# Performance work log

Hardware: AMD Instinct MI355X
Metric: run time of the kernel (lower is better)

The kernel has to match this reference:

```python
import jax, jax.numpy as jnp
import numpy as np
from jax import lax

K_KNN = 20           # DGCNN default neighborhood size
SLOPE = 0.2          # LeakyReLU negative slope


def _leaky(x):
    return jnp.where(x >= 0, x, SLOPE * x)


def _knn(x, k):
    # x: [B, N, C] -> idx [B, N, k] of nearest neighbors (incl. self) in feature space
    xx = jnp.sum(x * x, axis=-1)                       # [B, N]
    d = xx[:, :, None] + xx[:, None, :] - 2.0 * jnp.einsum('bnc,bmc->bnm', x, x)
    return lax.top_k(-d, k)[1]                          # [B, N, k]


def _edge_conv(x, idx, w, b):
    # x: [B, N, C]; idx: [B, N, k]; w: [O, 2C]; b: [O]
    neigh = jax.vmap(lambda xt, i: xt[i])(x, idx)       # [B, N, k, C]
    center = jnp.broadcast_to(x[:, :, None, :], neigh.shape)
    feat = jnp.concatenate([neigh - center, center], axis=-1)  # [B, N, k, 2C]
    h = _leaky(jnp.einsum('bnkc,oc->bnko', feat, w) + b)
    return jnp.max(h, axis=2)                           # [B, N, O]


def setup_inputs() -> dict:
    key = jax.random.key(0)
    ks = jax.random.split(key, 20)
    B, N, J, KR = 4, 4096, 24, 4
    layers = [64, 128, 256]

    def w_init(k, o, i):
        return jax.random.normal(k, (o, i), jnp.float32) / np.sqrt(i)

    inp = {
        'V': jax.random.normal(ks[0], (B, N, 3), jnp.float32),
        'W': jax.random.uniform(ks[1], (B, J, N), jnp.float32),
        'skeletonOneRingIdx': jax.random.randint(ks[2], (B, J, KR), 0, J),
    }
    # geoNet edge-conv params (input channels per layer: 3, 64, 128 -> 2C inputs)
    inp['g1_w'] = w_init(ks[3], 64, 6);    inp['g1_b'] = jnp.zeros((64,), jnp.float32)
    inp['g2_w'] = w_init(ks[4], 128, 128); inp['g2_b'] = jnp.zeros((128,), jnp.float32)
    inp['g3_w'] = w_init(ks[5], 256, 256); inp['g3_b'] = jnp.zeros((256,), jnp.float32)
    # skeleton edge-conv params (inputs: 451 -> 902, 256 -> 512, 128 -> 256)
    inp['s1_w'] = w_init(ks[6], 256, 902); inp['s1_b'] = jnp.zeros((256,), jnp.float32)
    inp['s2_w'] = w_init(ks[7], 128, 512); inp['s2_b'] = jnp.zeros((128,), jnp.float32)
    inp['s3_w'] = w_init(ks[8], 64, 256);  inp['s3_b'] = jnp.zeros((64,), jnp.float32)
    # jointMLP 1x1 convs: 448 -> 512 -> 256 -> 3
    inp['m1_w'] = w_init(ks[9], 512, 448);  inp['m1_b'] = jnp.zeros((512,), jnp.float32)
    inp['m2_w'] = w_init(ks[10], 256, 512); inp['m2_b'] = jnp.zeros((256,), jnp.float32)
    inp['m3_w'] = w_init(ks[11], 3, 256);   inp['m3_b'] = jnp.zeros((3,), jnp.float32)
    return inp


def reference(V, W, skeletonOneRingIdx,
              g1_w, g1_b, g2_w, g2_b, g3_w, g3_b,
              s1_w, s1_b, s2_w, s2_b, s3_w, s3_b,
              m1_w, m1_b, m2_w, m2_b, m3_w, m3_b):
    # ---- geoNet: DGCNN with dynamic kNN, output cat([xyz, l1, l2, l3]) -> [B, N, 451]
    outs = [V]
    h = V
    for w, b in ((g1_w, g1_b), (g2_w, g2_b), (g3_w, g3_b)):
        idx = _knn(h, K_KNN)
        h = _edge_conv(h, idx, w, b)
        outs.append(h)
    feat = jnp.concatenate(outs, axis=-1)                # [B, N, 451]

    # ---- weighted pooling onto skeleton joints
    pooled = jnp.einsum('bjn,bnc->bjc', W, feat)
    pooled = pooled / (jnp.sum(W, axis=-1, keepdims=True) + 1e-5)  # [B, J, 451]

    # ---- skeleton edge convs with fixed one-ring idx
    v1 = _edge_conv(pooled, skeletonOneRingIdx, s1_w, s1_b)  # [B, J, 256]
    v2 = _edge_conv(v1, skeletonOneRingIdx, s2_w, s2_b)      # [B, J, 128]
    v3 = _edge_conv(v2, skeletonOneRingIdx, s3_w, s3_b)      # [B, J, 64]

    joints = jnp.concatenate([v1, v2, v3], axis=-1)          # [B, J, 448]
    h = _leaky(jnp.einsum('bjc,oc->bjo', joints, m1_w) + m1_b)
    h = _leaky(jnp.einsum('bjc,oc->bjo', h, m2_w) + m2_b)
    out = jnp.einsum('bjc,oc->bjo', h, m3_w) + m3_b          # [B, J, 3]
    return out
```

## Files before the change

### kernel.cpp

```cpp
#include <hip/hip_runtime.h>
#include <hip/hip_bf16.h>
#include <float.h>

#define B_   4
#define N_   4096
#define J_   24
#define KR_  4
#define KNN_ 20
#define SLOPE 0.2f
#define SLABN 64
#define NSLAB (N_ / SLABN)
#define NTILE 32
#define SCAP 512

__global__ void k_norm(const float* __restrict__ h, float* __restrict__ xx, int C) {
    int i = blockIdx.x * blockDim.x + threadIdx.x;
    if (i >= B_ * N_) return;
    const float* hp = h + (size_t)i * C;
    float s = 0.f;
    for (int c = 0; c < C; ++c) { float v = hp[c]; s += v * v; }
    xx[i] = s;
}

__device__ __forceinline__ unsigned mapf(float f) {
    unsigned u = __float_as_uint(f);
    return (u & 0x80000000u) ? ~u : (u | 0x80000000u);
}
__device__ __forceinline__ unsigned key16(float f) {
    return mapf(f) >> 16;
}

__global__ __launch_bounds__(256) void k_dist(const float* __restrict__ Xall, int C,
                                              const float* __restrict__ xxall,
                                              unsigned short* __restrict__ Dall, int b0) {
    __shared__ float As[16][132];
    __shared__ float Bs[16][132];
    int b = b0 + blockIdx.y;
    const float* X   = Xall + (size_t)b * N_ * C;
    const float* xxb = xxall + (size_t)b * N_;
    unsigned short* D = Dall + (size_t)blockIdx.y * N_ * N_;

    int t = blockIdx.x;
    int ti = 0;
    while (t >= NTILE - ti) { t -= NTILE - ti; ++ti; }
    int tj = ti + t;
    int row0 = ti * 128, col0 = tj * 128;
    int tid = threadIdx.x;
    int tr = tid >> 4, tc = tid & 15;
    float acc[8][8] = {{0.f}};
    for (int kt = 0; kt < C; kt += 16) {
#pragma unroll
        for (int i = 0; i < 8; ++i) {
            int e = tid + 256 * i;
            int r = e >> 4, kk = e & 15;
            int gk = kt + kk;
            As[kk][r] = (gk < C) ? X[(size_t)(row0 + r) * C + gk] : 0.f;
            Bs[kk][r] = (gk < C) ? X[(size_t)(col0 + r) * C + gk] : 0.f;
        }
        __syncthreads();
#pragma unroll
        for (int kk = 0; kk < 16; ++kk) {
            float a[8], bv[8];
            *(float4*)&a[0]  = *(const float4*)&As[kk][tr * 4];
            *(float4*)&a[4]  = *(const float4*)&As[kk][64 + tr * 4];
            *(float4*)&bv[0] = *(const float4*)&Bs[kk][tc * 4];
            *(float4*)&bv[4] = *(const float4*)&Bs[kk][64 + tc * 4];
#pragma unroll
            for (int i = 0; i < 8; ++i)
#pragma unroll
                for (int j = 0; j < 8; ++j) acc[i][j] += a[i] * bv[j];
        }
        __syncthreads();
    }
    float xc[8], xr[8];
#pragma unroll
    for (int j = 0; j < 4; ++j) {
        xc[j]     = xxb[col0 + tc * 4 + j];
        xc[4 + j] = xxb[col0 + 64 + tc * 4 + j];
        xr[j]     = xxb[row0 + tr * 4 + j];
        xr[4 + j] = xxb[row0 + 64 + tr * 4 + j];
    }
#pragma unroll
    for (int i = 0; i < 8; ++i) {
        int lr = (i < 4) ? (tr * 4 + i) : (64 + tr * 4 + (i - 4));
        float xri = xr[i];
        float o0x = xri + xc[0] - 2.f * acc[i][0];
        float o0y = xri + xc[1] - 2.f * acc[i][1];
        float o0z = xri + xc[2] - 2.f * acc[i][2];
        float o0w = xri + xc[3] - 2.f * acc[i][3];
        float o1x = xri + xc[4] - 2.f * acc[i][4];
        float o1y = xri + xc[5] - 2.f * acc[i][5];
        float o1z = xri + xc[6] - 2.f * acc[i][6];
        float o1w = xri + xc[7] - 2.f * acc[i][7];
        unsigned short* dp = D + (size_t)(row0 + lr) * N_ + col0;
        uint2 w0, w1;
        w0.x = key16(o0x) | (key16(o0y) << 16);
        w0.y = key16(o0z) | (key16(o0w) << 16);
        w1.x = key16(o1x) | (key16(o1y) << 16);
        w1.y = key16(o1z) | (key16(o1w) << 16);
        *(uint2*)(dp + tc * 4)      = w0;
        *(uint2*)(dp + 64 + tc * 4) = w1;
    }
    if (ti == tj) return;
    float* tb = &As[0][0];
    for (int p = 0; p < 4; ++p) {
        __syncthreads();
        int h = p >> 1;
        int tclo = (p & 1) * 8;
        if (tc >= tclo && tc < tclo + 8) {
#pragma unroll
            for (int jj = 0; jj < 4; ++jj) {
                int j = h * 4 + jj;
                int cl = h * 64 + tc * 4 + jj - 32 * p;
                float xcj = xc[j];
                float4 vlo, vhi;
                vlo.x = xr[0] + xcj - 2.f * acc[0][j];
                vlo.y = xr[1] + xcj - 2.f * acc[1][j];
                vlo.z = xr[2] + xcj - 2.f * acc[2][j];
                vlo.w = xr[3] + xcj - 2.f * acc[3][j];
                vhi.x = xr[4] + xcj - 2.f * acc[4][j];
                vhi.y = xr[5] + xcj - 2.f * acc[5][j];
                vhi.z = xr[6] + xcj - 2.f * acc[6][j];
                vhi.w = xr[7] + xcj - 2.f * acc[7][j];
                *(float4*)&tb[cl * 132 + tr * 4]      = vlo;
                *(float4*)&tb[cl * 132 + 64 + tr * 4] = vhi;
            }
        }
        __syncthreads();
        int rl  = tid >> 3;
        int c16 = (tid & 7) * 16;
#pragma unroll
        for (int q = 0; q < 4; ++q) {
            float4 v = *(const float4*)&tb[rl * 132 + c16 + q * 4];
            uint2 ks;
            ks.x = key16(v.x) | (key16(v.y) << 16);
            ks.y = key16(v.z) | (key16(v.w) << 16);
            *(uint2*)(D + (size_t)(col0 + 32 * p + rl) * N_ + row0 + c16 + q * 4) = ks;
        }
    }
}

__device__ __forceinline__ unsigned long long shflx64(unsigned long long v, int m) {
    unsigned lo = (unsigned)v, hi = (unsigned)(v >> 32);
    lo = (unsigned)__shfl_xor((int)lo, m, 64);
    hi = (unsigned)__shfl_xor((int)hi, m, 64);
    return ((unsigned long long)hi << 32) | lo;
}

__device__ __forceinline__ float bsort64f(float v, int lane) {
#pragma unroll
    for (int k = 2; k <= 64; k <<= 1) {
#pragma unroll
        for (int j = k >> 1; j > 0; j >>= 1) {
            float o = __shfl_xor(v, j, 64);
            bool keepmin = (((lane & j) == 0) == ((lane & k) == 0));
            float mn = fminf(v, o), mx = fmaxf(v, o);
            v = keepmin ? mn : mx;
        }
    }
    return v;
}

__device__ __forceinline__ unsigned bsort64i(unsigned v, int lane) {
#pragma unroll
    for (int k = 2; k <= 64; k <<= 1) {
#pragma unroll
        for (int j = k >> 1; j > 0; j >>= 1) {
            unsigned o = (unsigned)__shfl_xor((int)v, j, 64);
            bool keepmin = (((lane & j) == 0) == ((lane & k) == 0));
            unsigned mn = (v < o) ? v : o;
            unsigned mx = (v < o) ? o : v;
            v = keepmin ? mn : mx;
        }
    }
    return v;
}

__device__ __forceinline__ unsigned long long bsort64u(unsigned long long v, int lane) {
#pragma unroll
    for (int k = 2; k <= 64; k <<= 1) {
#pragma unroll
        for (int j = k >> 1; j > 0; j >>= 1) {
            unsigned long long o = shflx64(v, j);
            bool keepmin = (((lane & j) == 0) == ((lane & k) == 0));
            bool oless = o < v;
            unsigned long long mn = oless ? o : v;
            unsigned long long mx = oless ? v : o;
            v = keepmin ? mn : mx;
        }
    }
    return v;
}

__global__ __launch_bounds__(256) void k_sel(const unsigned short* __restrict__ Dall,
                                             const float* __restrict__ Xall, int C,
                                             const float* __restrict__ xxall,
                                             int* __restrict__ knnIdx, int b0) {
    __shared__ unsigned sidx[SCAP];
    __shared__ unsigned long long skey[SCAP];
    __shared__ float qf[128];
    __shared__ unsigned stau[4];
    __shared__ int scnt;
    int b = b0 + blockIdx.y;
    const unsigned short* Db = Dall + (size_t)blockIdx.y * N_ * N_;
    const float* Xb  = Xall + (size_t)b * N_ * C;
    const float* xxb = xxall + (size_t)b * N_;
    int* idxout = knnIdx + (size_t)b * N_ * KNN_;
    int ql   = blockIdx.x;
    int wv   = threadIdx.x >> 6;
    int lane = threadIdx.x & 63;
    int gbase = wv * 1024 + lane * 16;
    if (threadIdx.x == 0) scnt = 0;
    for (int c = threadIdx.x; c < C; c += 256) qf[c] = Xb[(size_t)ql * C + c];

    const uint4* kp = (const uint4*)(Db + (size_t)ql * N_ + gbase);
    uint4 pa = kp[0], pb = kp[1];
    unsigned kv[16];
    kv[0] = pa.x & 0xffffu;  kv[1] = pa.x >> 16;
    kv[2] = pa.y & 0xffffu;  kv[3] = pa.y >> 16;
    kv[4] = pa.z & 0xffffu;  kv[5] = pa.z >> 16;
    kv[6] = pa.w & 0xffffu;  kv[7] = pa.w >> 16;
    kv[8] = pb.x & 0xffffu;  kv[9] = pb.x >> 16;
    kv[10] = pb.y & 0xffffu; kv[11] = pb.y >> 16;
    kv[12] = pb.z & 0xffffu; kv[13] = pb.z >> 16;
    kv[14] = pb.w & 0xffffu; kv[15] = pb.w >> 16;

    unsigned mn = kv[0];
#pragma unroll
    for (int t = 1; t < 16; ++t) mn = (kv[t] < mn) ? kv[t] : mn;
    mn = bsort64i(mn, lane);
    unsigned tw = (unsigned)__shfl((int)mn, 19, 64);
    if (lane == 0) stau[wv] = tw;
    __syncthreads();
    unsigned tau = stau[0];
    tau = (stau[1] < tau) ? stau[1] : tau;
    tau = (stau[2] < tau) ? stau[2] : tau;
    tau = (stau[3] < tau) ? stau[3] : tau;

#pragma unroll
    for (int t = 0; t < 16; ++t) {
        if (kv[t] <= tau) {
            int p = atomicAdd(&scnt, 1);
            if (p < SCAP) sidx[p] = (unsigned)(gbase + t);
        }
    }
    __syncthreads();
    int S = scnt; if (S > SCAP) S = SCAP;
    float xxq = xxb[ql];
    const float4* xq4 = (const float4*)qf;
    for (int s = threadIdx.x; s < S; s += 256) {
        int j = (int)sidx[s];
        const float4* xj = (const float4*)(Xb + (size_t)j * C);
        float a0 = 0.f, a1 = 0.f, a2 = 0.f, a3 = 0.f;
        for (int c4 = 0; c4 < (C >> 2); ++c4) {
            float4 x = xj[c4]; float4 qv = xq4[c4];
            a0 = fmaf(qv.x, x.x, a0);
            a1 = fmaf(qv.y, x.y, a1);
            a2 = fmaf(qv.z, x.z, a2);
            a3 = fmaf(qv.w, x.w, a3);
        }
        float dot = (a0 + a1) + (a2 + a3);
        float d = xxq + xxb[j] - 2.f * dot;
        skey[s] = ((unsigned long long)mapf(d) << 32) | (unsigned)j;
    }
    __syncthreads();
    if (wv != 0) return;
    unsigned long long key = (lane < S) ? skey[lane] : ~0ull;
    key = bsort64u(key, lane);
    for (int consumed = 64; consumed < S; consumed += 44) {
        if (lane >= 20) {
            int src = consumed + lane - 20;
            key = (src < S) ? skey[src] : ~0ull;
        }
        key = bsort64u(key, lane);
    }
    if (lane < KNN_) idxout[ql * KNN_ + lane] = (int)(unsigned)key;
}

__global__ __launch_bounds__(256) void k_selC3(const float* __restrict__ V,
                                               const float* __restrict__ xx,
                                               int* __restrict__ knnIdx) {
    __shared__ unsigned long long sbuf[SCAP];
    __shared__ float stau[4];
    __shared__ int scnt;
    int b    = blockIdx.y;
    const float* Xb  = V + (size_t)b * N_ * 3;
    const float* xxb = xx + (size_t)b * N_;
    int* idxout = knnIdx + (size_t)b * N_ * KNN_;
    int q    = blockIdx.x;
    int wv   = threadIdx.x >> 6;
    int lane = threadIdx.x & 63;
    int gbase = wv * 1024 + lane * 16;
    if (threadIdx.x == 0) scnt = 0;

    float qx = Xb[q * 3], qy = Xb[q * 3 + 1], qz = Xb[q * 3 + 2];
    float xxq = xxb[q];

    float pts[48];
    const float4* src = (const float4*)(Xb + (size_t)gbase * 3);
#pragma unroll
    for (int t = 0; t < 12; ++t) ((float4*)pts)[t] = src[t];

    float dv[16];
#pragma unroll
    for (int t = 0; t < 16; ++t) {
        float dot = qx * pts[3 * t];
        dot = fmaf(qy, pts[3 * t + 1], dot);
        dot = fmaf(qz, pts[3 * t + 2], dot);
        dv[t] = xxq + xxb[gbase + t] - 2.f * dot;
    }

    float mn = dv[0];
#pragma unroll
    for (int t = 1; t < 16; ++t) mn = fminf(mn, dv[t]);
    mn = bsort64f(mn, lane);
    float tw = __shfl(mn, 19, 64);
    if (lane == 0) stau[wv] = tw;
    __syncthreads();
    float tau = fminf(fminf(stau[0], stau[1]), fminf(stau[2], stau[3]));

#pragma unroll
    for (int t = 0; t < 16; ++t) {
        if (dv[t] <= tau) {
            int p = atomicAdd(&scnt, 1);
            if (p < SCAP)
                sbuf[p] = ((unsigned long long)mapf(dv[t]) << 32) | (unsigned)(gbase + t);
        }
    }
    __syncthreads();
    if (wv != 0) return;
    int S = scnt; if (S > SCAP) S = SCAP;
    unsigned long long key = (lane < S) ? sbuf[lane] : ~0ull;
    key = bsort64u(key, lane);
    for (int consumed = 64; consumed < S; consumed += 44) {
        if (lane >= 20) {
            int srci = consumed + lane - 20;
            key = (srci < S) ? sbuf[srci] : ~0ull;
        }
        key = bsort64u(key, lane);
    }
    if (lane < KNN_) idxout[q * KNN_ + lane] = (int)(unsigned)key;
}

__device__ __forceinline__ void prepP_elem(const float* __restrict__ w,
                                           const float* __restrict__ bias,
                                           int C, int O, float* __restrict__ P,
                                           float* __restrict__ b2, int i) {
    int O2 = 2 * O;
    if (i < O2) b2[i] = (i < O) ? 0.f : bias[i - O];
    if (i >= C * O2) return;
    int k = i / O2, col = i % O2;
    float v;
    if (col < O) v = w[(size_t)col * 2 * C + k];
    else { int o = col - O; v = w[(size_t)o * 2 * C + C + k] - w[(size_t)o * 2 * C + k]; }
    P[i] = v;
}
__device__ __forceinline__ void transp_elem(const float* __restrict__ w, int O, int K,
                                            float* __restrict__ wT, int i) {
    if (i >= O * K) return;
    int k = i / O, o = i % O;
    wT[i] = w[(size_t)o * K + k];
}

__global__ void k_prepall(const float* g1w, const float* g1b,
                          const float* g2w, const float* g2b,
                          const float* g3w, const float* g3b,
                          const float* s1w, const float* s1b,
                          const float* s2w, const float* s2b,
                          const float* s3w, const float* s3b,
                          const float* m1w, const float* m2w, const float* m3w,
                          float* P1, float* P2, float* P3, float* P4, float* P5,
                          float* P6, float* P7, float* P8, float* P9,
                          float* bb1, float* bb2, float* bb3,
                          float* bb4, float* bb5, float* bb6) {
    int i = blockIdx.x * 256 + threadIdx.x;
    switch (blockIdx.y) {
        case 0: prepP_elem(g1w, g1b, 3,   64,  P1, bb1, i); break;
        case 1: prepP_elem(g2w, g2b, 64,  128, P2, bb2, i); break;
        case 2: prepP_elem(g3w, g3b, 128, 256, P3, bb3, i); break;
        case 3: prepP_elem(s1w, s1b, 451, 256, P4, bb4, i); break;
        case 4: prepP_elem(s2w, s2b, 256, 128, P5, bb5, i); break;
        case 5: prepP_elem(s3w, s3b, 128, 64,  P6, bb6, i); break;
        case 6: transp_elem(m1w, 512, 448, P7, i); break;
        case 7: transp_elem(m2w, 256, 512, P8, i); break;
        case 8: transp_elem(m3w, 3,   256, P9, i); break;
    }
}

__global__ __launch_bounds__(256) void k_gemm(const float* __restrict__ A, int lda,
                                              const float* __restrict__ Bm,
                                              float* __restrict__ Cm, int ldc,
                                              int M, int N, int K,
                                              const float* __restrict__ bias, int leaky) {
    __shared__ float As[16][68];
    __shared__ float Bs[16][68];
    int tid = threadIdx.x;
    int row0 = blockIdx.y * 64, col0 = blockIdx.x * 64;
    int tr = tid >> 4, tc = tid & 15;
    float acc[4][4] = {{0.f}};
    for (int kt = 0; kt < K; kt += 16) {
#pragma unroll
        for (int i = 0; i < 4; ++i) {
            int e = tid + 256 * i;
            int r = e >> 4, kk = e & 15;
            int gr = row0 + r, gk = kt + kk;
            float v = 0.f;
            if (gr < M && gk < K) v = A[(size_t)gr * lda + gk];
            As[kk][r] = v;
        }
#pragma unroll
        for (int i = 0; i < 4; ++i) {
            int e = tid + 256 * i;
            int kk = e >> 6, c = e & 63;
            int gk = kt + kk, gc = col0 + c;
            float v = 0.f;
            if (gk < K && gc < N) v = Bm[(size_t)gk * N + gc];
            Bs[kk][c] = v;
        }
        __syncthreads();
#pragma unroll
        for (int kk = 0; kk < 16; ++kk) {
            float a[4], bv[4];
            *(float4*)&a[0]  = *(const float4*)&As[kk][tr * 4];
            *(float4*)&bv[0] = *(const float4*)&Bs[kk][tc * 4];
#pragma unroll
            for (int i = 0; i < 4; ++i)
#pragma unroll
                for (int j = 0; j < 4; ++j) acc[i][j] += a[i] * bv[j];
        }
        __syncthreads();
    }
#pragma unroll
    for (int i = 0; i < 4; ++i) {
        int r = row0 + tr * 4 + i;
        if (r >= M) continue;
#pragma unroll
        for (int j = 0; j < 4; ++j) {
            int c = col0 + tc * 4 + j;
            if (c >= N) continue;
            float v = acc[i][j];
            if (bias) v += bias[c];
            if (leaky) v = v >= 0.f ? v : SLOPE * v;
            Cm[(size_t)r * ldc + c] = v;
        }
    }
}

__global__ __launch_bounds__(256) void k_sgemm(const float* __restrict__ A, int lda,
                                               const float* __restrict__ Bm,
                                               float* __restrict__ Cm, int ldc,
                                               int N, int K,
                                               const float* __restrict__ bias, int leaky) {
    extern __shared__ float Arow[];
    int r   = blockIdx.x;
    int c0  = blockIdx.y * 256;
    int tid = threadIdx.x;
    for (int k = tid; k < K; k += 256) Arow[k] = A[(size_t)r * lda + k];
    __syncthreads();
    int c = c0 + tid;
    if (c >= N) return;
    float acc = bias ? bias[c] : 0.f;
    for (int k = 0; k < K; ++k) acc += Arow[k] * Bm[(size_t)k * N + c];
    if (leaky) acc = acc >= 0.f ? acc : SLOPE * acc;
    Cm[(size_t)r * ldc + c] = acc;
}

__global__ void k_gathermax(const float* __restrict__ Y, int O, int R,
                            const int* __restrict__ idx, int kc,
                            float* __restrict__ out, int ldo, int ooff,
                            float* __restrict__ xxout) {
    extern __shared__ int sidx[];
    __shared__ float red[256];
    int br = blockIdx.x;
    int b  = br / R;
    int o  = threadIdx.x;
    if (o < kc) sidx[o] = idx[(size_t)br * kc + o];
    __syncthreads();
    int O2 = 2 * O;
    float z = Y[(size_t)br * O2 + O + o];
    float best = -FLT_MAX;
    for (int k = 0; k < kc; ++k) {
        int m = sidx[k];
        best = fmaxf(best, Y[(size_t)(b * R + m) * O2 + o]);
    }
    float r = z + best;
    r = r >= 0.f ? r : SLOPE * r;
    out[(size_t)br * ldo + ooff + o] = r;
    if (xxout) {
        red[o] = r * r;
        __syncthreads();
        for (int s = blockDim.x >> 1; s > 0; s >>= 1) {
            if (o < s) red[o] += red[o + s];
            __syncthreads();
        }
        if (o == 0) xxout[br] = red[0];
    }
}

__device__ __forceinline__ void chan_map(int b, int c,
                                         const float* Vf, const float* l1,
                                         const float* l2, const float* l3,
                                         const float*& p, int& st) {
    if (c < 3)        { st = 3;   p = Vf + (size_t)b * N_ * 3   + c; }
    else if (c < 67)  { st = 64;  p = l1 + (size_t)b * N_ * 64  + (c - 3); }
    else if (c < 195) { st = 128; p = l2 + (size_t)b * N_ * 128 + (c - 67); }
    else              { st = 256; p = l3 + (size_t)b * N_ * 256 + (c - 195); }
}

__global__ __launch_bounds__(256) void k_pool2(const float* __restrict__ Vf,
                                               const float* __restrict__ l1,
                                               const float* __restrict__ l2,
                                               const float* __restrict__ l3,
                                               const float* __restrict__ W,
                                               float* __restrict__ ppool,
                                               float* __restrict__ psw) {
    __shared__ float Wl[SLABN][J_];
    int blk  = blockIdx.x;
    int b    = blk / NSLAB, slab = blk % NSLAB;
    int n0   = slab * SLABN;
    int tid  = threadIdx.x;

    for (int e = tid; e < J_ * SLABN; e += 256) {
        int j = e / SLABN, n = e % SLABN;
        Wl[n][j] = W[((size_t)b * J_ + j) * N_ + n0 + n];
    }
    __syncthreads();

    if (tid < J_) {
        float s = 0.f;
        for (int n = 0; n < SLABN; ++n) s += Wl[n][tid];
        psw[(size_t)blk * J_ + tid] = s;
    }

    int c0 = tid, c1 = tid + 256;
    const float *p0, *p1 = nullptr; int s0, s1 = 0;
    chan_map(b, c0, Vf, l1, l2, l3, p0, s0);
    bool has1 = (c1 < 451);
    if (has1) chan_map(b, c1, Vf, l1, l2, l3, p1, s1);

    float acc0[J_], acc1[J_];
#pragma unroll
    for (int j = 0; j < J_; ++j) { acc0[j] = 0.f; acc1[j] = 0.f; }

    for (int n = 0; n < SLABN; ++n) {
        float v0 = p0[(size_t)(n0 + n) * s0];
        float v1 = has1 ? p1[(size_t)(n0 + n) * s1] : 0.f;
        const float* wn = &Wl[n][0];
#pragma unroll
        for (int q = 0; q < J_ / 4; ++q) {
            float4 w4 = *(const float4*)(wn + 4 * q);
            acc0[4*q+0] += w4.x * v0;  acc1[4*q+0] += w4.x * v1;
            acc0[4*q+1] += w4.y * v0;  acc1[4*q+1] += w4.y * v1;
            acc0[4*q+2] += w4.z * v0;  acc1[4*q+2] += w4.z * v1;
            acc0[4*q+3] += w4.w * v0;  acc1[4*q+3] += w4.w * v1;
        }
    }
    float* pp = ppool + (size_t)blk * J_ * 451;
#pragma unroll
    for (int j = 0; j < J_; ++j) {
        pp[(size_t)j * 451 + c0] = acc0[j];
        if (has1) pp[(size_t)j * 451 + c1] = acc1[j];
    }
}

__global__ __launch_bounds__(256) void k_poolred(const float* __restrict__ ppool,
                                                 const float* __restrict__ psw,
                                                 float* __restrict__ pooled) {
    int bj = blockIdx.x;
    int b  = bj / J_, j = bj % J_;
    int tid = threadIdx.x;

    float sw = 0.f;
    for (int sl = 0; sl < NSLAB; ++sl) sw += psw[(size_t)(b * NSLAB + sl) * J_ + j];
    float inv = 1.f / (sw + 1e-5f);

    for (int c = tid; c < 451; c += 256) {
        float s = 0.f;
        for (int sl = 0; sl < NSLAB; ++sl)
            s += ppool[((size_t)(b * NSLAB + sl) * J_ + j) * 451 + c];
        pooled[(size_t)bj * 451 + c] = s * inv;
    }
}

extern "C" void kernel_launch(void* const* d_in, const int* in_sizes, int n_in,
                              void* d_out, int out_size, void* d_ws, size_t ws_size,
                              hipStream_t stream) {
    const float* V  = (const float*)d_in[0];
    const float* W  = (const float*)d_in[1];
    const int* ringIdx = (const int*)d_in[2];
    const float* g1w = (const float*)d_in[3];
    const float* g1b = (const float*)d_in[4];
    const float* g2w = (const float*)d_in[5];
    const float* g2b = (const float*)d_in[6];
    const float* g3w = (const float*)d_in[7];
    const float* g3b = (const float*)d_in[8];
    const float* s1w = (const float*)d_in[9];
    const float* s1b = (const float*)d_in[10];
    const float* s2w = (const float*)d_in[11];
    const float* s2b = (const float*)d_in[12];
    const float* s3w = (const float*)d_in[13];
    const float* s3b = (const float*)d_in[14];
    const float* m1w = (const float*)d_in[15];
    const float* m1b = (const float*)d_in[16];
    const float* m2w = (const float*)d_in[17];
    const float* m2b = (const float*)d_in[18];
    const float* m3w = (const float*)d_in[19];
    const float* m3b = (const float*)d_in[20];
    (void)n_in; (void)in_sizes; (void)out_size;

    const int szP1 = 3 * 128,    szP2 = 64 * 256,  szP3 = 128 * 512;
    const int szP4 = 451 * 512,  szP5 = 256 * 256, szP6 = 128 * 128;
    const int szP7 = 448 * 512,  szP8 = 512 * 256, szP9 = 256 * 3;

    auto dreg_floats = [&](int nd) -> size_t {
        size_t a = (size_t)nd * ((size_t)N_ * N_ / 2);
        size_t ymax = (size_t)B_ * N_ * 512;
        size_t pool = (size_t)B_ * NSLAB * J_ * 451 + (size_t)B_ * NSLAB * J_;
        size_t r = a;
        if (ymax > r) r = ymax;
        if (pool > r) r = pool;
        return r;
    };
    auto layout_bytes = [&](int nd) -> size_t {
        size_t f = 0;
        f += (size_t)B_ * N_ * 64 + (size_t)B_ * N_ * 128 + (size_t)B_ * N_ * 256;
        f += (size_t)B_ * N_;
        f += dreg_floats(nd);
        f += (size_t)B_ * N_ * KNN_;
        f += (size_t)B_ * J_ * 451 + (size_t)B_ * J_ * 448;
        f += (size_t)B_ * J_ * 512 + (size_t)B_ * J_ * 256;
        f += (size_t)(szP1 + szP2 + szP3 + szP4 + szP5 + szP6 + szP7 + szP8 + szP9);
        f += 128 + 256 + 512 + 512 + 256 + 128;
        return f * 4;
    };
    int nb = 1;
    if (ws_size >= layout_bytes(4)) nb = 4;
    else if (ws_size >= layout_bytes(2)) nb = 2;

    float* ws = (float*)d_ws;
    size_t off = 0;
    float* l1 = ws + off; off += (size_t)B_ * N_ * 64;
    float* l2 = ws + off; off += (size_t)B_ * N_ * 128;
    float* l3 = ws + off; off += (size_t)B_ * N_ * 256;
    float* xx = ws + off; off += (size_t)B_ * N_;
    float* D  = ws + off; off += dreg_floats(nb);
    unsigned short* Dk = (unsigned short*)D;
    float* Y  = D;
    float* ppool = D;
    float* psw   = D + (size_t)B_ * NSLAB * J_ * 451;
    int* knnIdx = (int*)(ws + off); off += (size_t)B_ * N_ * KNN_;
    float* pooled = ws + off; off += (size_t)B_ * J_ * 451;
    float* joints = ws + off; off += (size_t)B_ * J_ * 448;
    float* h1 = ws + off; off += (size_t)B_ * J_ * 512;
    float* h2 = ws + off; off += (size_t)B_ * J_ * 256;
    float* P1 = ws + off; off += szP1;
    float* P2 = ws + off; off += szP2;
    float* P3 = ws + off; off += szP3;
    float* P4 = ws + off; off += szP4;
    float* P5 = ws + off; off += szP5;
    float* P6 = ws + off; off += szP6;
    float* P7 = ws + off; off += szP7;
    float* P8 = ws + off; off += szP8;
    float* P9 = ws + off; off += szP9;
    float* bb1 = ws + off; off += 128;
    float* bb2 = ws + off; off += 256;
    float* bb3 = ws + off; off += 512;
    float* bb4 = ws + off; off += 512;
    float* bb5 = ws + off; off += 256;
    float* bb6 = ws + off; off += 128;

    const int M = B_ * N_;
    const int MJ = B_ * J_;
    const int NUTRI = NTILE * (NTILE + 1) / 2;

    k_prepall<<<dim3((szP4 + 255) / 256, 9), 256, 0, stream>>>(
        g1w, g1b, g2w, g2b, g3w, g3b, s1w, s1b, s2w, s2b, s3w, s3b,
        m1w, m2w, m3w, P1, P2, P3, P4, P5, P6, P7, P8, P9,
        bb1, bb2, bb3, bb4, bb5, bb6);

    k_norm<<<(M + 255) / 256, 256, 0, stream>>>(V, xx, 3);
    k_selC3<<<dim3(N_, B_), 256, 0, stream>>>(V, xx, knnIdx);
    k_gemm<<<dim3(2, M / 64), 256, 0, stream>>>(V, 3, P1, Y, 128, M, 128, 3, bb1, 0);
    k_gathermax<<<M, 64, KNN_ * sizeof(int), stream>>>(Y, 64, N_, knnIdx, KNN_, l1, 64, 0, xx);

    for (int g = 0; g < B_; g += nb) {
        k_dist<<<dim3(NUTRI, nb), 256, 0, stream>>>(l1, 64, xx, Dk, g);
        k_sel<<<dim3(N_, nb), 256, 0, stream>>>(Dk, l1, 64, xx, knnIdx, g);
    }
    k_gemm<<<dim3(4, M / 64), 256, 0, stream>>>(l1, 64, P2, Y, 256, M, 256, 64, bb2, 0);
    k_gathermax<<<M, 128, KNN_ * sizeof(int), stream>>>(Y, 128, N_, knnIdx, KNN_, l2, 128, 0, xx);

    for (int g = 0; g < B_; g += nb) {
        k_dist<<<dim3(NUTRI, nb), 256, 0, stream>>>(l2, 128, xx, Dk, g);
        k_sel<<<dim3(N_, nb), 256, 0, stream>>>(Dk, l2, 128, xx, knnIdx, g);
    }
    k_gemm<<<dim3(8, M / 64), 256, 0, stream>>>(l2, 128, P3, Y, 512, M, 512, 128, bb3, 0);
    k_gathermax<<<M, 256, KNN_ * sizeof(int), stream>>>(Y, 256, N_, knnIdx, KNN_, l3, 256, 0, nullptr);

    k_pool2<<<B_ * NSLAB, 256, 0, stream>>>(V, l1, l2, l3, W, ppool, psw);
    k_poolred<<<MJ, 256, 0, stream>>>(ppool, psw, pooled);

    k_sgemm<<<dim3(MJ, 2), 256, 451 * sizeof(float), stream>>>(pooled, 451, P4, Y, 512, 512, 451, bb4, 0);
    k_gathermax<<<MJ, 256, KR_ * sizeof(int), stream>>>(Y, 256, J_, ringIdx, KR_, joints, 448, 0, nullptr);

    k_sgemm<<<dim3(MJ, 1), 256, 256 * sizeof(float), stream>>>(joints, 448, P5, Y, 256, 256, 256, bb5, 0);
    k_gathermax<<<MJ, 128, KR_ * sizeof(int), stream>>>(Y, 128, J_, ringIdx, KR_, joints, 448, 256, nullptr);

    k_sgemm<<<dim3(MJ, 1), 256, 128 * sizeof(float), stream>>>(joints + 256, 448, P6, Y, 128, 128, 128, bb6, 0);
    k_gathermax<<<MJ, 64, KR_ * sizeof(int), stream>>>(Y, 64, J_, ringIdx, KR_, joints, 448, 384, nullptr);

    k_sgemm<<<dim3(MJ, 2), 256, 448 * sizeof(float), stream>>>(joints, 448, P7, h1, 512, 512, 448, m1b, 1);
    k_sgemm<<<dim3(MJ, 1), 256, 512 * sizeof(float), stream>>>(h1, 512, P8, h2, 256, 256, 512, m2b, 1);
    k_sgemm<<<dim3(MJ, 1), 256, 256 * sizeof(float), stream>>>(h2, 256, P9, (float*)d_out, 3, 3, 256, m3b, 0);
}
```

Before: 995.8 us.

## Compute kNN distance tiles with split-bf16 MFMA instead of fp32 FMA

Features are split into bf16 hi/lo halves by a new kernel, and the pairwise dot products in k_dist are computed with three bf16 MFMA products per fragment (hi*hi, hi*lo, lo*hi) to approximate fp32 accuracy on matrix cores. The output tile is staged in shared memory as 16-bit keys and written row-wise and transposed with vector stores. To absorb the small precision loss, the selection threshold gets a slack and the candidate capacity grows. The cost is extra split passes, more workspace, and a larger candidate set for the exact refinement.

```diff
diff --git a/kernel.cpp b/kernel.cpp
--- a/kernel.cpp
+++ b/kernel.cpp
@@ -11,7 +11,11 @@
 #define SLABN 64
 #define NSLAB (N_ / SLABN)
 #define NTILE 32
-#define SCAP 512
+#define SCAP 768
+#define KSLACK 8u
+
+typedef __attribute__((ext_vector_type(8))) short bf16x8;
+typedef __attribute__((ext_vector_type(4))) float f32x4;
 
 __global__ void k_norm(const float* __restrict__ h, float* __restrict__ xx, int C) {
     int i = blockIdx.x * blockDim.x + threadIdx.x;
@@ -30,13 +34,41 @@
     return mapf(f) >> 16;
 }
 
-__global__ __launch_bounds__(256) void k_dist(const float* __restrict__ Xall, int C,
+__global__ void k_split(const float* __restrict__ h, unsigned short* __restrict__ hi,
+                        unsigned short* __restrict__ lo, int total4) {
+    int i = blockIdx.x * 256 + threadIdx.x;
+    if (i >= total4) return;
+    float4 v = ((const float4*)h)[i];
+    ushort4 h4, l4;
+    {
+        unsigned u = __float_as_uint(v.x); h4.x = (unsigned short)(u >> 16);
+        float r = v.x - __uint_as_float(u & 0xffff0000u); l4.x = (unsigned short)(__float_as_uint(r) >> 16);
+    }
+    {
+        unsigned u = __float_as_uint(v.y); h4.y = (unsigned short)(u >> 16);
+        float r = v.y - __uint_as_float(u & 0xffff0000u); l4.y = (unsigned short)(__float_as_uint(r) >> 16);
+    }
+    {
+        unsigned u = __float_as_uint(v.z); h4.z = (unsigned short)(u >> 16);
+        float r = v.z - __uint_as_float(u & 0xffff0000u); l4.z = (unsigned short)(__float_as_uint(r) >> 16);
+    }
+    {
+        unsigned u = __float_as_uint(v.w); h4.w = (unsigned short)(u >> 16);
+        float r = v.w - __uint_as_float(u & 0xffff0000u); l4.w = (unsigned short)(__float_as_uint(r) >> 16);
+    }
+    ((ushort4*)hi)[i] = h4;
+    ((ushort4*)lo)[i] = l4;
+}
+
+__global__ __launch_bounds__(256) void k_dist(const unsigned short* __restrict__ Hi,
+                                              const unsigned short* __restrict__ Lo,
+                                              int C,
                                               const float* __restrict__ xxall,
                                               unsigned short* __restrict__ Dall, int b0) {
-    __shared__ float As[16][132];
-    __shared__ float Bs[16][132];
+    __shared__ unsigned short tile[128][136];
     int b = b0 + blockIdx.y;
-    const float* X   = Xall + (size_t)b * N_ * C;
+    const unsigned short* XH = Hi + (size_t)b * N_ * C;
+    const unsigned short* XL = Lo + (size_t)b * N_ * C;
     const float* xxb = xxall + (size_t)b * N_;
     unsigned short* D = Dall + (size_t)blockIdx.y * N_ * N_;
 
@@ -45,97 +77,79 @@
     while (t >= NTILE - ti) { t -= NTILE - ti; ++ti; }
     int tj = ti + t;
     int row0 = ti * 128, col0 = tj * 128;
-    int tid = threadIdx.x;
-    int tr = tid >> 4, tc = tid & 15;
-    float acc[8][8] = {{0.f}};
-    for (int kt = 0; kt < C; kt += 16) {
-#pragma unroll
-        for (int i = 0; i < 8; ++i) {
-            int e = tid + 256 * i;
-            int r = e >> 4, kk = e & 15;
-            int gk = kt + kk;
-            As[kk][r] = (gk < C) ? X[(size_t)(row0 + r) * C + gk] : 0.f;
-            Bs[kk][r] = (gk < C) ? X[(size_t)(col0 + r) * C + gk] : 0.f;
-        }
-        __syncthreads();
-#pragma unroll
-        for (int kk = 0; kk < 16; ++kk) {
-            float a[8], bv[8];
-            *(float4*)&a[0]  = *(const float4*)&As[kk][tr * 4];
-            *(float4*)&a[4]  = *(const float4*)&As[kk][64 + tr * 4];
-            *(float4*)&bv[0] = *(const float4*)&Bs[kk][tc * 4];
-            *(float4*)&bv[4] = *(const float4*)&Bs[kk][64 + tc * 4];
-#pragma unroll
-            for (int i = 0; i < 8; ++i)
-#pragma unroll
-                for (int j = 0; j < 8; ++j) acc[i][j] += a[i] * bv[j];
-        }
-        __syncthreads();
-    }
-    float xc[8], xr[8];
-#pragma unroll
-    for (int j = 0; j < 4; ++j) {
-        xc[j]     = xxb[col0 + tc * 4 + j];
-        xc[4 + j] = xxb[col0 + 64 + tc * 4 + j];
-        xr[j]     = xxb[row0 + tr * 4 + j];
-        xr[4 + j] = xxb[row0 + 64 + tr * 4 + j];
-    }
-#pragma unroll
-    for (int i = 0; i < 8; ++i) {
-        int lr = (i < 4) ? (tr * 4 + i) : (64 + tr * 4 + (i - 4));
-        float xri = xr[i];
-        float o0x = xri + xc[0] - 2.f * acc[i][0];
-        float o0y = xri + xc[1] - 2.f * acc[i][1];
-        float o0z = xri + xc[2] - 2.f * acc[i][2];
-        float o0w = xri + xc[3] - 2.f * acc[i][3];
-        float o1x = xri + xc[4] - 2.f * acc[i][4];
-        float o1y = xri + xc[5] - 2.f * acc[i][5];
-        float o1z = xri + xc[6] - 2.f * acc[i][6];
-        float o1w = xri + xc[7] - 2.f * acc[i][7];
-        unsigned short* dp = D + (size_t)(row0 + lr) * N_ + col0;
-        uint2 w0, w1;
-        w0.x = key16(o0x) | (key16(o0y) << 16);
-        w0.y = key16(o0z) | (key16(o0w) << 16);
-        w1.x = key16(o1x) | (key16(o1y) << 16);
-        w1.y = key16(o1z) | (key16(o1w) << 16);
-        *(uint2*)(dp + tc * 4)      = w0;
-        *(uint2*)(dp + 64 + tc * 4) = w1;
+    int tid  = threadIdx.x;
+    int wv   = tid >> 6, lane = tid & 63;
+    int wr   = wv >> 1,  wc   = wv & 1;
+    int rbase = row0 + wr * 64;
+    int cbase = col0 + wc * 64;
+    int lp    = lane & 15;
+    int kgrp  = lane >> 4;
+
+    f32x4 acc[4][4];
+#pragma unroll
+    for (int i = 0; i < 4; ++i)
+#pragma unroll
+        for (int j = 0; j < 4; ++j) acc[i][j] = (f32x4){0.f, 0.f, 0.f, 0.f};
+
+    for (int ks = 0; ks < C; ks += 32) {
+        int kb = ks + kgrp * 8;
+        bf16x8 ah[4], al[4];
+#pragma unroll
+        for (int fi = 0; fi < 4; ++fi) {
+            size_t ro = (size_t)(rbase + fi * 16 + lp) * C + kb;
+            ah[fi] = *(const bf16x8*)(XH + ro);
+            al[fi] = *(const bf16x8*)(XL + ro);
+        }
+#pragma unroll
+        for (int fj = 0; fj < 4; ++fj) {
+            size_t co = (size_t)(cbase + fj * 16 + lp) * C + kb;
+            bf16x8 bh = *(const bf16x8*)(XH + co);
+            bf16x8 bl = *(const bf16x8*)(XL + co);
+#pragma unroll
+            for (int fi = 0; fi < 4; ++fi) {
+                acc[fi][fj] = __builtin_amdgcn_mfma_f32_16x16x32_bf16(ah[fi], bh, acc[fi][fj], 0, 0, 0);
+                acc[fi][fj] = __builtin_amdgcn_mfma_f32_16x16x32_bf16(ah[fi], bl, acc[fi][fj], 0, 0, 0);
+                acc[fi][fj] = __builtin_amdgcn_mfma_f32_16x16x32_bf16(al[fi], bh, acc[fi][fj], 0, 0, 0);
+            }
+        }
+    }
+
+    float xxrv = xxb[rbase + lane];
+    float xxcv = xxb[cbase + lane];
+    int rsub = (lane >> 4) * 4;
+#pragma unroll
+    for (int fi = 0; fi < 4; ++fi) {
+#pragma unroll
+        for (int fj = 0; fj < 4; ++fj) {
+            float xc = __shfl(xxcv, fj * 16 + lp, 64);
+#pragma unroll
+            for (int r = 0; r < 4; ++r) {
+                float xr = __shfl(xxrv, fi * 16 + rsub + r, 64);
+                float d = xr + xc - 2.f * acc[fi][fj][r];
+                tile[wr * 64 + fi * 16 + rsub + r][wc * 64 + fj * 16 + lp] =
+                    (unsigned short)key16(d);
+            }
+        }
+    }
+    __syncthreads();
+
+    {
+        int row = tid >> 1, seg = (tid & 1) * 64;
+        const uint4* src = (const uint4*)&tile[row][seg];
+        uint4* dst = (uint4*)(D + (size_t)(row0 + row) * N_ + col0 + seg);
+#pragma unroll
+        for (int q = 0; q < 8; ++q) dst[q] = src[q];
     }
     if (ti == tj) return;
-    float* tb = &As[0][0];
-    for (int p = 0; p < 4; ++p) {
-        __syncthreads();
-        int h = p >> 1;
-        int tclo = (p & 1) * 8;
-        if (tc >= tclo && tc < tclo + 8) {
-#pragma unroll
-            for (int jj = 0; jj < 4; ++jj) {
-                int j = h * 4 + jj;
-                int cl = h * 64 + tc * 4 + jj - 32 * p;
-                float xcj = xc[j];
-                float4 vlo, vhi;
-                vlo.x = xr[0] + xcj - 2.f * acc[0][j];
-                vlo.y = xr[1] + xcj - 2.f * acc[1][j];
-                vlo.z = xr[2] + xcj - 2.f * acc[2][j];
-                vlo.w = xr[3] + xcj - 2.f * acc[3][j];
-                vhi.x = xr[4] + xcj - 2.f * acc[4][j];
-                vhi.y = xr[5] + xcj - 2.f * acc[5][j];
-                vhi.z = xr[6] + xcj - 2.f * acc[6][j];
-                vhi.w = xr[7] + xcj - 2.f * acc[7][j];
-                *(float4*)&tb[cl * 132 + tr * 4]      = vlo;
-                *(float4*)&tb[cl * 132 + 64 + tr * 4] = vhi;
-            }
-        }
-        __syncthreads();
-        int rl  = tid >> 3;
-        int c16 = (tid & 7) * 16;
-#pragma unroll
-        for (int q = 0; q < 4; ++q) {
-            float4 v = *(const float4*)&tb[rl * 132 + c16 + q * 4];
-            uint2 ks;
-            ks.x = key16(v.x) | (key16(v.y) << 16);
-            ks.y = key16(v.z) | (key16(v.w) << 16);
-            *(uint2*)(D + (size_t)(col0 + 32 * p + rl) * N_ + row0 + c16 + q * 4) = ks;
+    {
+        int c = tid >> 1, rseg = (tid & 1) * 64;
+        unsigned short* dst = D + (size_t)(col0 + c) * N_ + row0 + rseg;
+#pragma unroll
+        for (int q8 = 0; q8 < 8; ++q8) {
+            unsigned short s[8];
+#pragma unroll
+            for (int q = 0; q < 8; ++q) s[q] = tile[rseg + q8 * 8 + q][c];
+            *(uint4*)(dst + q8 * 8) = *(const uint4*)s;
         }
     }
 }
@@ -236,6 +250,8 @@
     tau = (stau[1] < tau) ? stau[1] : tau;
     tau = (stau[2] < tau) ? stau[2] : tau;
     tau = (stau[3] < tau) ? stau[3] : tau;
+    tau += KSLACK;
+    if (tau > 0xffffu) tau = 0xffffu;
 
 #pragma unroll
     for (int t = 0; t < 16; ++t) {
@@ -626,6 +642,7 @@
         f += (size_t)B_ * N_ * 64 + (size_t)B_ * N_ * 128 + (size_t)B_ * N_ * 256;
         f += (size_t)B_ * N_;
         f += dreg_floats(nd);
+        f += 2 * ((size_t)B_ * N_ * 128 / 2);
         f += (size_t)B_ * N_ * KNN_;
         f += (size_t)B_ * J_ * 451 + (size_t)B_ * J_ * 448;
         f += (size_t)B_ * J_ * 512 + (size_t)B_ * J_ * 256;
@@ -648,6 +665,8 @@
     float* Y  = D;
     float* ppool = D;
     float* psw   = D + (size_t)B_ * NSLAB * J_ * 451;
+    unsigned short* Xhi = (unsigned short*)(ws + off); off += (size_t)B_ * N_ * 128 / 2;
+    unsigned short* Xlo = (unsigned short*)(ws + off); off += (size_t)B_ * N_ * 128 / 2;
     int* knnIdx = (int*)(ws + off); off += (size_t)B_ * N_ * KNN_;
     float* pooled = ws + off; off += (size_t)B_ * J_ * 451;
     float* joints = ws + off; off += (size_t)B_ * J_ * 448;
@@ -683,15 +702,17 @@
     k_gemm<<<dim3(2, M / 64), 256, 0, stream>>>(V, 3, P1, Y, 128, M, 128, 3, bb1, 0);
     k_gathermax<<<M, 64, KNN_ * sizeof(int), stream>>>(Y, 64, N_, knnIdx, KNN_, l1, 64, 0, xx);
 
+    k_split<<<(M * 64 / 4 + 255) / 256, 256, 0, stream>>>(l1, Xhi, Xlo, M * 64 / 4);
     for (int g = 0; g < B_; g += nb) {
-        k_dist<<<dim3(NUTRI, nb), 256, 0, stream>>>(l1, 64, xx, Dk, g);
+        k_dist<<<dim3(NUTRI, nb), 256, 0, stream>>>(Xhi, Xlo, 64, xx, Dk, g);
         k_sel<<<dim3(N_, nb), 256, 0, stream>>>(Dk, l1, 64, xx, knnIdx, g);
     }
     k_gemm<<<dim3(4, M / 64), 256, 0, stream>>>(l1, 64, P2, Y, 256, M, 256, 64, bb2, 0);
     k_gathermax<<<M, 128, KNN_ * sizeof(int), stream>>>(Y, 128, N_, knnIdx, KNN_, l2, 128, 0, xx);
 
+    k_split<<<(M * 128 / 4 + 255) / 256, 256, 0, stream>>>(l2, Xhi, Xlo, M * 128 / 4);
     for (int g = 0; g < B_; g += nb) {
-        k_dist<<<dim3(NUTRI, nb), 256, 0, stream>>>(l2, 128, xx, Dk, g);
+        k_dist<<<dim3(NUTRI, nb), 256, 0, stream>>>(Xhi, Xlo, 128, xx, Dk, g);
         k_sel<<<dim3(N_, nb), 256, 0, stream>>>(Dk, l2, 128, xx, knnIdx, g);
     }
     k_gemm<<<dim3(8, M / 64), 256, 0, stream>>>(l2, 128, P3, Y, 512, M, 512, 128, bb3, 0);
```

After: 946.5 us. 5.0% less time.
